# Performance work log

Hardware: AMD Instinct MI355X
Metric: run time of the kernel (lower is better)

The kernel has to match this reference:

```python
import jax, jax.numpy as jnp
import numpy as np
import math

HEADS = 16


def setup_inputs() -> dict:
    key = jax.random.key(0)
    kx, kq, kk, kv = jax.random.split(key, 4)
    B, S, E = 2, 2048, 1024
    x = jax.random.normal(kx, (B, S, E), dtype=jnp.float32)
    # torch nn.Linear weights are [out, in]; y = x @ W.T
    Wq = jax.random.normal(kq, (E, E), dtype=jnp.float32) * (1.0 / math.sqrt(E))
    Wk = jax.random.normal(kk, (E, E), dtype=jnp.float32) * (1.0 / math.sqrt(E))
    Wv = jax.random.normal(kv, (E, E), dtype=jnp.float32) * (1.0 / math.sqrt(E))
    # multiplicative causal mask, as the module applies mask by elementwise multiply
    mask = jnp.tril(jnp.ones((S, S), dtype=jnp.float32))
    return {"x": x, "Wq": Wq, "Wk": Wk, "Wv": Wv, "mask": mask}


def reference(x, Wq, Wk, Wv, mask):
    B, S, E = x.shape
    H = HEADS
    D = E // H
    q = (x @ Wq.T).reshape(B, S, H, D)
    k = (x @ Wk.T).reshape(B, S, H, D)
    v = (x @ Wv.T).reshape(B, S, H, D)
    # scores: [B, H, S, S]
    sim = jnp.einsum('nqhd,nkhd->nhqk', q, k)
    sim = sim * mask  # multiplicative mask, broadcast over (B, H)
    # NOTE: original scales by sqrt(emsize), not sqrt(head_dim)
    attn = jax.nn.softmax(sim / math.sqrt(E), axis=-1)
    out = jnp.einsum('nhql,nlhd->nqhd', attn, v).reshape(B, S, E)
    return out
```

## Files before the change

kernel.cpp:

```cpp
#include <hip/hip_runtime.h>
#include <hip/hip_bf16.h>
#include <cstdint>

using bf16   = __bf16;
using bf16x4 = __attribute__((ext_vector_type(4))) __bf16;
using bf16x8 = __attribute__((ext_vector_type(8))) __bf16;
using f32x4  = __attribute__((ext_vector_type(4))) float;

#define MFMA16(a, b, c) __builtin_amdgcn_mfma_f32_16x16x32_bf16((a), (b), (c), 0, 0, 0)

__device__ __forceinline__ void load_lds16(const bf16* g, bf16* l) {
    __builtin_amdgcn_global_load_lds(
        (const __attribute__((address_space(1))) void*)g,
        (__attribute__((address_space(3))) void*)l, 16, 0, 0);
}

__global__ __launch_bounds__(256) void cast_all(const float* __restrict__ x,
                                                const float* __restrict__ Wq,
                                                const float* __restrict__ Wk,
                                                const float* __restrict__ Wv,
                                                bf16* __restrict__ xb,
                                                bf16* __restrict__ wb,
                                                float qscale) {
    int i = blockIdx.x * 256 + threadIdx.x;
    const float* src; bf16* dst; int off; float scale = 1.0f;
    if (i < 1048576)      { src = x;  dst = xb;              off = i; }
    else if (i < 1310720) { src = Wq; dst = wb;              off = i - 1048576; scale = qscale; }
    else if (i < 1572864) { src = Wk; dst = wb + (1u << 20); off = i - 1310720; }
    else                  { src = Wv; dst = wb + (2u << 20); off = i - 1572864; }
    float4 v = reinterpret_cast<const float4*>(src)[off];
    bf16x4 o;
    o[0] = (bf16)(v.x * scale); o[1] = (bf16)(v.y * scale);
    o[2] = (bf16)(v.z * scale); o[3] = (bf16)(v.w * scale);
    reinterpret_cast<bf16x4*>(dst)[off] = o;
}

__global__ __launch_bounds__(256) void qkv_gemm(const bf16* __restrict__ xb,
                                                const bf16* __restrict__ wb,
                                                bf16* __restrict__ Qo,
                                                bf16* __restrict__ Ko,
                                                bf16* __restrict__ Vt) {
    const int n0 = blockIdx.x * 128;
    const int m0 = blockIdx.y * 128;

    __shared__ __align__(16) bf16 As[128 * 64];
    __shared__ __align__(16) bf16 Bs[128 * 64];

    const int t    = threadIdx.x;
    const int lane = t & 63;
    const int wid  = t >> 6;
    const int quad = lane >> 4;
    const int col  = lane & 15;
    const int wm   = wid & 1;
    const int wn   = wid >> 1;

    const int rsub = lane >> 3;
    const int csw  = ((lane & 7) ^ rsub) * 8;

    f32x4 acc[4][4] = {};

    const bf16* Ag = &xb[(size_t)(m0 + rsub) * 1024 + csw];
    const bf16* Bg = &wb[(size_t)(n0 + rsub) * 1024 + csw];

    for (int kc = 0; kc < 1024; kc += 64) {
        __syncthreads();
#pragma unroll
        for (int j = 0; j < 4; ++j) {
            const int c = wid * 4 + j;
            load_lds16(Ag + kc + (size_t)c * 8 * 1024, &As[c * 512]);
        }
#pragma unroll
        for (int j = 0; j < 4; ++j) {
            const int c = wid * 4 + j;
            load_lds16(Bg + kc + (size_t)c * 8 * 1024, &Bs[c * 512]);
        }
        __syncthreads();

#pragma unroll
        for (int ks = 0; ks < 2; ++ks) {
            const int ca = ((ks * 4 + quad) ^ (col & 7)) * 8;
            bf16x8 a[4], b[4];
#pragma unroll
            for (int i = 0; i < 4; ++i)
                a[i] = *reinterpret_cast<const bf16x8*>(
                    &As[(wm * 64 + i * 16 + col) * 64 + ca]);
#pragma unroll
            for (int i = 0; i < 4; ++i)
                b[i] = *reinterpret_cast<const bf16x8*>(
                    &Bs[(wn * 64 + i * 16 + col) * 64 + ca]);
#pragma unroll
            for (int mt = 0; mt < 4; ++mt)
#pragma unroll
                for (int nt = 0; nt < 4; ++nt)
                    acc[mt][nt] = MFMA16(a[mt], b[nt], acc[mt][nt]);
        }
    }

    const int w = blockIdx.x >> 3;
#pragma unroll
    for (int mt = 0; mt < 4; ++mt) {
#pragma unroll
        for (int nt = 0; nt < 4; ++nt) {
#pragma unroll
            for (int r = 0; r < 4; ++r) {
                int m = m0 + wm * 64 + mt * 16 + quad * 4 + r;
                int n = n0 + wn * 64 + nt * 16 + col;
                int bb = m >> 11, s = m & 2047;
                int n1 = n & 1023;
                int h = n1 >> 6, d = n1 & 63;
                size_t bh = (size_t)(bb * 16 + h);
                bf16 v = (bf16)acc[mt][nt][r];
                if (w == 0)      Qo[(bh * 2048 + s) * 64 + d] = v;
                else if (w == 1) Ko[(bh * 2048 + s) * 64 + d] = v;
                else             Vt[(bh * 64 + d) * 2048 + s] = v;
            }
        }
    }
}

__global__ __launch_bounds__(256) void tail_kernel(const bf16* __restrict__ Vt,
                                                   float* __restrict__ Tail) {
    const int bh = blockIdx.x;
    const bf16* Vg = Vt + (size_t)bh * 64 * 2048;
    float* Tg = Tail + (size_t)bh * 33 * 64;

    __shared__ float ts[64 * 33];
    const int tid = threadIdx.x;

#pragma unroll
    for (int i = 0; i < 8; ++i) {
        int task = i * 256 + tid;
        int d = task >> 5, tt = task & 31;
        const bf16* p = &Vg[(size_t)d * 2048 + tt * 64];
        float s = 0.0f;
#pragma unroll
        for (int j = 0; j < 8; ++j) {
            bf16x8 v = *reinterpret_cast<const bf16x8*>(p + j * 8);
#pragma unroll
            for (int e = 0; e < 8; ++e) s += (float)v[e];
        }
        ts[d * 33 + tt] = s;
    }
    __syncthreads();

    if (tid < 64) {
        const int d = tid;
        float s = 0.0f;
        Tg[32 * 64 + d] = 0.0f;
        for (int tt = 31; tt >= 1; --tt) {
            s += ts[d * 33 + tt];
            Tg[tt * 64 + d] = s;
        }
    }
}

__global__ __launch_bounds__(256) void attn_kernel(const bf16* __restrict__ Q,
                                                   const bf16* __restrict__ K,
                                                   const bf16* __restrict__ Vt,
                                                   const float* __restrict__ Tail,
                                                   float* __restrict__ out) {
    const int b = blockIdx.z;
    const int h = blockIdx.y;
    const int j  = ((blockIdx.y >> 3) ^ blockIdx.z) & 1;
    const int qt = j ? (31 - (int)blockIdx.x) : (int)blockIdx.x;
    const int q0 = qt * 64;
    const int np = (qt >> 1) + 1;

    const int t    = threadIdx.x;
    const int lane = t & 63;
    const int wid  = t >> 6;
    const int quad = lane >> 4;
    const int col  = lane & 15;

    const int bh = b * 16 + h;
    const bf16* Qg = Q + (size_t)bh * 2048 * 64;
    const bf16* Kg = K + (size_t)bh * 2048 * 64;
    const bf16* Vg = Vt + (size_t)bh * 64 * 2048;

    __shared__ __align__(16) bf16 Ks[128 * 64];
    __shared__ __align__(16) bf16 Vs[64 * 128];
    __shared__ __align__(16) bf16 Ps[4 * 16 * 72];
    bf16* Pw = &Ps[wid * 16 * 72];

    bf16x8 qf[2];
#pragma unroll
    for (int ks = 0; ks < 2; ++ks)
        qf[ks] = *reinterpret_cast<const bf16x8*>(
            &Qg[(size_t)(q0 + wid * 16 + col) * 64 + ks * 32 + quad * 8]);

    bf16x8 ones;
#pragma unroll
    for (int i = 0; i < 8; ++i) ones[i] = (bf16)1.0f;

    f32x4 o[4];
    f32x4 la;
    {
        const float tc = 64.0f * (float)(32 - 2 * np);
#pragma unroll
        for (int r = 0; r < 4; ++r) la[r] = tc;
        const float* Tg = Tail + ((size_t)bh * 33 + 2 * np) * 64;
#pragma unroll
        for (int dt = 0; dt < 4; ++dt) {
            float tv = Tg[dt * 16 + col];
#pragma unroll
            for (int r = 0; r < 4; ++r) o[dt][r] = tv;
        }
    }

    const int qrow = q0 + wid * 16 + quad * 4;
    const int rsubK = lane >> 3;
    const int cswK  = ((lane & 7) ^ rsubK) * 8;
    const int rV    = lane >> 4;
    const int ccV   = lane & 15;

    const int s0max = (np - 1) * 128;

    for (int s0 = 0; s0 < np * 128; s0 += 128) {
        __syncthreads();
#pragma unroll
        for (int jj = 0; jj < 4; ++jj) {
            const int c = wid * 4 + jj;
            load_lds16(&Kg[(size_t)(s0 + c * 8 + rsubK) * 64 + cswK], &Ks[c * 512]);
            const int d = c * 4 + rV;
            load_lds16(&Vg[(size_t)d * 2048 + s0 + ((ccV ^ (d & 15)) * 8)], &Vs[c * 512]);
        }
        __syncthreads();

        f32x4 sv[8] = {};
#pragma unroll
        for (int ks = 0; ks < 2; ++ks) {
            const int ca = ((ks * 4 + quad) ^ (col & 7)) * 8;
#pragma unroll
            for (int nt = 0; nt < 8; ++nt) {
                bf16x8 kb = *reinterpret_cast<const bf16x8*>(
                    &Ks[(nt * 16 + col) * 64 + ca]);
                sv[nt] = MFMA16(qf[ks], kb, sv[nt]);
            }
        }

        if (s0 == s0max) {
#pragma unroll
            for (int nt = 0; nt < 8; ++nt) {
                int kidx = s0 + nt * 16 + col;
#pragma unroll
                for (int r = 0; r < 4; ++r)
                    if (kidx > qrow + r) sv[nt][r] = 0.0f;
            }
        }

#pragma unroll
        for (int hh = 0; hh < 2; ++hh) {
#pragma unroll
            for (int nt = 0; nt < 4; ++nt)
#pragma unroll
                for (int r = 0; r < 4; ++r)
                    Pw[(quad * 4 + r) * 72 + nt * 16 + col] =
                        (bf16)__builtin_amdgcn_exp2f(sv[hh * 4 + nt][r]);

#pragma unroll
            for (int gg = 0; gg < 2; ++gg) {
                bf16x8 pa = *reinterpret_cast<const bf16x8*>(
                    &Pw[col * 72 + gg * 32 + quad * 8]);
                la = MFMA16(pa, ones, la);
                const int g = hh * 2 + gg;
#pragma unroll
                for (int dt = 0; dt < 4; ++dt) {
                    bf16x8 vb = *reinterpret_cast<const bf16x8*>(
                        &Vs[(dt * 16 + col) * 128 + ((g * 4 + quad) ^ col) * 8]);
                    o[dt] = MFMA16(pa, vb, o[dt]);
                }
            }
        }
    }

#pragma unroll
    for (int r = 0; r < 4; ++r) {
        int q = qrow + r;
        float inv = __builtin_amdgcn_rcpf(la[r]);
#pragma unroll
        for (int dt = 0; dt < 4; ++dt) {
            int d = dt * 16 + col;
            out[((size_t)b * 2048 + q) * 1024 + h * 64 + d] = o[dt][r] * inv;
        }
    }
}

extern "C" void kernel_launch(void* const* d_in, const int* in_sizes, int n_in,
                              void* d_out, int out_size, void* d_ws, size_t ws_size,
                              hipStream_t stream) {
    const float* x  = (const float*)d_in[0];
    const float* Wq = (const float*)d_in[1];
    const float* Wk = (const float*)d_in[2];
    const float* Wv = (const float*)d_in[3];
    float* out = (float*)d_out;

    char* ws = (char*)d_ws;
    bf16*  xb   = (bf16*)(ws);
    bf16*  wb   = (bf16*)(ws + (size_t)(8  << 20));
    bf16*  Qb   = (bf16*)(ws + (size_t)(14 << 20));
    bf16*  Kb   = (bf16*)(ws + (size_t)(22 << 20));
    bf16*  Vtb  = (bf16*)(ws + (size_t)(30 << 20));
    float* Tail = (float*)(ws + (size_t)(38 << 20));

    const float QSCALE = 1.44269504088896f / 32.0f;

    cast_all<<<7168, 256, 0, stream>>>(x, Wq, Wk, Wv, xb, wb, QSCALE);

    qkv_gemm<<<dim3(24, 32), 256, 0, stream>>>(xb, wb, Qb, Kb, Vtb);

    tail_kernel<<<32, 256, 0, stream>>>(Vtb, Tail);

    attn_kernel<<<dim3(32, 16, 2), 256, 0, stream>>>(Qb, Kb, Vtb, Tail, out);
}
```

Before: 183.8 us.

## Split attention waves 2x2 over query and key halves with shared P tile

Reorganizes the attention block so the four waves form a 2x2 grid. Each wave covers 32 query rows and one 64-key half for QK^T, and one 32-column half of the head dimension for PV. The probability tile is now written to a shared 64x136 LDS buffer and read by all waves after an extra barrier, so each wave reuses its K and V fragments across two query sub-tiles. It also transposes the S MFMA operands so exp outputs can be stored as packed bf16x4, and raises wave priority around the MFMA phases. The trade-off is an extra __syncthreads per key tile, a larger LDS footprint, and redundant row-sum MFMAs in the two kh waves.

```diff
diff --git a/kernel.cpp b/kernel.cpp
--- a/kernel.cpp
+++ b/kernel.cpp
@@ -171,6 +171,8 @@
     const int wid  = t >> 6;
     const int quad = lane >> 4;
     const int col  = lane & 15;
+    const int qh   = wid & 1;
+    const int kh   = wid >> 1;
 
     const int bh = b * 16 + h;
     const bf16* Qg = Q + (size_t)bh * 2048 * 64;
@@ -179,35 +181,39 @@
 
     __shared__ __align__(16) bf16 Ks[128 * 64];
     __shared__ __align__(16) bf16 Vs[64 * 128];
-    __shared__ __align__(16) bf16 Ps[4 * 16 * 72];
-    bf16* Pw = &Ps[wid * 16 * 72];
-
-    bf16x8 qf[2];
-#pragma unroll
-    for (int ks = 0; ks < 2; ++ks)
-        qf[ks] = *reinterpret_cast<const bf16x8*>(
-            &Qg[(size_t)(q0 + wid * 16 + col) * 64 + ks * 32 + quad * 8]);
+    __shared__ __align__(16) bf16 Ps[64 * 136];
+
+    bf16x8 qf[2][2];
+#pragma unroll
+    for (int qs = 0; qs < 2; ++qs)
+#pragma unroll
+        for (int ks = 0; ks < 2; ++ks)
+            qf[qs][ks] = *reinterpret_cast<const bf16x8*>(
+                &Qg[(size_t)(q0 + qh * 32 + qs * 16 + col) * 64 + ks * 32 + quad * 8]);
 
     bf16x8 ones;
 #pragma unroll
     for (int i = 0; i < 8; ++i) ones[i] = (bf16)1.0f;
 
-    f32x4 o[4];
-    f32x4 la;
+    f32x4 o[2][2];
+    f32x4 la[2];
     {
         const float tc = 64.0f * (float)(32 - 2 * np);
 #pragma unroll
-        for (int r = 0; r < 4; ++r) la[r] = tc;
+        for (int qs = 0; qs < 2; ++qs)
+#pragma unroll
+            for (int r = 0; r < 4; ++r) la[qs][r] = tc;
         const float* Tg = Tail + ((size_t)bh * 33 + 2 * np) * 64;
 #pragma unroll
-        for (int dt = 0; dt < 4; ++dt) {
-            float tv = Tg[dt * 16 + col];
-#pragma unroll
-            for (int r = 0; r < 4; ++r) o[dt][r] = tv;
-        }
-    }
-
-    const int qrow = q0 + wid * 16 + quad * 4;
+        for (int dt = 0; dt < 2; ++dt) {
+            float tv = Tg[kh * 32 + dt * 16 + col];
+#pragma unroll
+            for (int qs = 0; qs < 2; ++qs)
+#pragma unroll
+                for (int r = 0; r < 4; ++r) o[qs][dt][r] = tv;
+        }
+    }
+
     const int rsubK = lane >> 3;
     const int cswK  = ((lane & 7) ^ rsubK) * 8;
     const int rV    = lane >> 4;
@@ -226,61 +232,81 @@
         }
         __syncthreads();
 
-        f32x4 sv[8] = {};
+        f32x4 sv[2][4] = {};
+        __builtin_amdgcn_s_setprio(1);
 #pragma unroll
         for (int ks = 0; ks < 2; ++ks) {
             const int ca = ((ks * 4 + quad) ^ (col & 7)) * 8;
 #pragma unroll
-            for (int nt = 0; nt < 8; ++nt) {
+            for (int nt = 0; nt < 4; ++nt) {
                 bf16x8 kb = *reinterpret_cast<const bf16x8*>(
-                    &Ks[(nt * 16 + col) * 64 + ca]);
-                sv[nt] = MFMA16(qf[ks], kb, sv[nt]);
-            }
-        }
+                    &Ks[((kh * 4 + nt) * 16 + col) * 64 + ca]);
+                sv[0][nt] = MFMA16(kb, qf[0][ks], sv[0][nt]);
+                sv[1][nt] = MFMA16(kb, qf[1][ks], sv[1][nt]);
+            }
+        }
+        __builtin_amdgcn_s_setprio(0);
 
         if (s0 == s0max) {
 #pragma unroll
-            for (int nt = 0; nt < 8; ++nt) {
-                int kidx = s0 + nt * 16 + col;
+            for (int qs = 0; qs < 2; ++qs) {
+                const int qc = q0 + qh * 32 + qs * 16 + col;
+#pragma unroll
+                for (int nt = 0; nt < 4; ++nt)
+#pragma unroll
+                    for (int r = 0; r < 4; ++r) {
+                        int kidx = s0 + kh * 64 + nt * 16 + quad * 4 + r;
+                        if (kidx > qc) sv[qs][nt][r] = 0.0f;
+                    }
+            }
+        }
+
+#pragma unroll
+        for (int qs = 0; qs < 2; ++qs) {
+            bf16* Pq = &Ps[(qh * 32 + qs * 16 + col) * 136 + kh * 64];
+#pragma unroll
+            for (int nt = 0; nt < 4; ++nt) {
+                bf16x4 pw;
 #pragma unroll
                 for (int r = 0; r < 4; ++r)
-                    if (kidx > qrow + r) sv[nt][r] = 0.0f;
-            }
-        }
-
-#pragma unroll
-        for (int hh = 0; hh < 2; ++hh) {
-#pragma unroll
-            for (int nt = 0; nt < 4; ++nt)
-#pragma unroll
-                for (int r = 0; r < 4; ++r)
-                    Pw[(quad * 4 + r) * 72 + nt * 16 + col] =
-                        (bf16)__builtin_amdgcn_exp2f(sv[hh * 4 + nt][r]);
-
-#pragma unroll
-            for (int gg = 0; gg < 2; ++gg) {
-                bf16x8 pa = *reinterpret_cast<const bf16x8*>(
-                    &Pw[col * 72 + gg * 32 + quad * 8]);
-                la = MFMA16(pa, ones, la);
-                const int g = hh * 2 + gg;
-#pragma unroll
-                for (int dt = 0; dt < 4; ++dt) {
-                    bf16x8 vb = *reinterpret_cast<const bf16x8*>(
-                        &Vs[(dt * 16 + col) * 128 + ((g * 4 + quad) ^ col) * 8]);
-                    o[dt] = MFMA16(pa, vb, o[dt]);
-                }
-            }
-        }
-    }
-
-#pragma unroll
-    for (int r = 0; r < 4; ++r) {
-        int q = qrow + r;
-        float inv = __builtin_amdgcn_rcpf(la[r]);
-#pragma unroll
-        for (int dt = 0; dt < 4; ++dt) {
-            int d = dt * 16 + col;
-            out[((size_t)b * 2048 + q) * 1024 + h * 64 + d] = o[dt][r] * inv;
+                    pw[r] = (bf16)__builtin_amdgcn_exp2f(sv[qs][nt][r]);
+                *reinterpret_cast<bf16x4*>(&Pq[nt * 16 + quad * 4]) = pw;
+            }
+        }
+
+        __syncthreads();
+
+        __builtin_amdgcn_s_setprio(1);
+#pragma unroll
+        for (int kg = 0; kg < 4; ++kg) {
+            bf16x8 pa0 = *reinterpret_cast<const bf16x8*>(
+                &Ps[(qh * 32 + col) * 136 + kg * 32 + quad * 8]);
+            bf16x8 pa1 = *reinterpret_cast<const bf16x8*>(
+                &Ps[(qh * 32 + 16 + col) * 136 + kg * 32 + quad * 8]);
+            la[0] = MFMA16(pa0, ones, la[0]);
+            la[1] = MFMA16(pa1, ones, la[1]);
+#pragma unroll
+            for (int dt = 0; dt < 2; ++dt) {
+                bf16x8 vb = *reinterpret_cast<const bf16x8*>(
+                    &Vs[(kh * 32 + dt * 16 + col) * 128 + ((kg * 4 + quad) ^ col) * 8]);
+                o[0][dt] = MFMA16(pa0, vb, o[0][dt]);
+                o[1][dt] = MFMA16(pa1, vb, o[1][dt]);
+            }
+        }
+        __builtin_amdgcn_s_setprio(0);
+    }
+
+#pragma unroll
+    for (int qs = 0; qs < 2; ++qs) {
+#pragma unroll
+        for (int r = 0; r < 4; ++r) {
+            int q = q0 + qh * 32 + qs * 16 + quad * 4 + r;
+            float inv = __builtin_amdgcn_rcpf(la[qs][r]);
+#pragma unroll
+            for (int dt = 0; dt < 2; ++dt) {
+                int d = kh * 32 + dt * 16 + col;
+                out[((size_t)b * 2048 + q) * 1024 + h * 64 + d] = o[qs][dt][r] * inv;
+            }
         }
     }
 }
```

Result: faster. 177.1 us (-3.6%).
